# Kernel tuning notes

Hardware: AMD Instinct MI355X
Metric: run time of the kernel (lower is better)

Reference implementation:

```python
import jax, jax.numpy as jnp
import numpy as np
import math

E, NNODE = 32768, 2048          # edges, nodes
NUM_SPECIES, EMB = 100, 32
MUL, HIDDEN, N_RBF, LMAX, ENV_P = 16, 256, 8, 3, 6
SL = {0: slice(0, 1), 1: slice(1, 4), 2: slice(4, 9), 3: slice(9, 16)}  # SH blocks


def _cg(j1, m1, j2, m2, j3, m3):
    """Clebsch-Gordan coefficient (Racah formula), complex SH basis."""
    if m1 + m2 != m3:
        return 0.0
    f = math.factorial
    pre = math.sqrt((2*j3+1) * f(j1+j2-j3) * f(j1-j2+j3) * f(-j1+j2+j3) / f(j1+j2+j3+1))
    pre *= math.sqrt(f(j3+m3)*f(j3-m3)*f(j1-m1)*f(j1+m1)*f(j2-m2)*f(j2+m2))
    s = 0.0
    kmin = max(0, j2 - j3 - m1, j1 - j3 + m2)
    kmax = min(j1 + j2 - j3, j1 - m1, j2 + m2)
    for k in range(kmin, kmax + 1):
        s += (-1)**k / (f(k)*f(j1+j2-j3-k)*f(j1-m1-k)*f(j2+m2-k)*f(j3-j2+m1+k)*f(j3-j1-m2+k))
    return pre * s


def _umat(l):
    """Complex->real spherical-harmonics change of basis."""
    U = np.zeros((2*l+1, 2*l+1), dtype=complex)
    U[l, l] = 1.0
    s2 = 1.0 / math.sqrt(2.0)
    for m in range(1, l + 1):
        U[l+m, l-m] = s2
        U[l+m, l+m] = (-1)**m * s2
        U[l-m, l-m] = 1j * s2
        U[l-m, l+m] = -1j * (-1)**m * s2
    return U


def _real_coupling(l1, l2, l3):
    """Real-basis CG coupling tensor, Frobenius-normalized (w3j analogue)."""
    C = np.zeros((2*l1+1, 2*l2+1, 2*l3+1), dtype=complex)
    for a, m1 in enumerate(range(-l1, l1+1)):
        for b, m2 in enumerate(range(-l2, l2+1)):
            for c, m3 in enumerate(range(-l3, l3+1)):
                C[a, b, c] = _cg(l1, m1, l2, m2, l3, m3)
    T = np.einsum('am,bn,ck,mnk->abc', _umat(l1), _umat(l2), _umat(l3).conj(), C)
    Tr, Ti = np.real(T), np.imag(T)
    T = Tr if np.linalg.norm(Tr) >= np.linalg.norm(Ti) else Ti
    n = np.linalg.norm(T)
    return None if n < 1e-8 else (T / n).astype(np.float32)


PATHS = {l3: [] for l3 in range(LMAX + 1)}
for _l1 in range(LMAX + 1):
    for _l2 in range(LMAX + 1):
        for _l3 in range(abs(_l1 - _l2), min(_l1 + _l2, LMAX) + 1):
            _T = _real_coupling(_l1, _l2, _l3)
            if _T is not None:
                PATHS[_l3].append((_l1, _l2, jnp.asarray(_T)))
NPATH = {l3: len(PATHS[l3]) for l3 in range(LMAX + 1)}


def envelope(d):  # polynomial smoothing envelope, p=6, cutoff=1
    p = ENV_P
    e = 1.0 - 0.5*(p+1)*(p+2)*d**p + p*(p+2)*d**(p+1) - 0.5*p*(p+1)*d**(p+2)
    return jnp.where(d < 1.0, e, 0.0)


def bessel(d):  # radial Bessel basis [E] -> [E, N_RBF]
    n = jnp.arange(1, N_RBF + 1, dtype=d.dtype)
    ds = jnp.where(d == 0.0, 1.0, d)[:, None]
    return (math.sqrt(2.0) * jnp.sin(n * jnp.pi * ds) / ds) * envelope(d)[:, None]


def sph_harm16(u):  # real SH l=0..3, component norm (|Y_l|^2 = 2l+1), [E,16]
    x, y, z = u[:, 0], u[:, 1], u[:, 2]
    x2, y2, z2 = x*x, y*y, z*z
    s3, s15, s5 = math.sqrt(3.0), math.sqrt(15.0), math.sqrt(5.0)
    s358, s105 = math.sqrt(35.0/8.0), math.sqrt(105.0)
    s218, s7 = math.sqrt(21.0/8.0), math.sqrt(7.0)
    return jnp.stack([
        jnp.ones_like(x),
        s3*y, s3*z, s3*x,
        s15*x*y, s15*y*z, 0.5*s5*(3*z2 - 1), s15*x*z, 0.5*s15*(x2 - y2),
        s358*y*(3*x2 - y2), s105*x*y*z, s218*y*(5*z2 - 1), 0.5*s7*(5*z2 - 3)*z,
        s218*x*(5*z2 - 1), 0.5*s105*(x2 - y2)*z, s358*x*(x2 - y2),
    ], axis=1)


def dense(x, W):  # e3nn-style bias-free linear, 1/sqrt(fan_in)
    return (x @ W) / math.sqrt(W.shape[0])


def dense_axis(V, W):  # [E,C,K] x [C,D] -> [E,D,K]
    return jnp.einsum('eck,cd->edk', V, W) / math.sqrt(W.shape[0])


def tensor_product(A, B, lmax_out):
    """CG tensor product [E,MUL,16] x [E,MUL,16] -> {l3: [E,MUL*npath,2l3+1]}."""
    out = {}
    for l3 in range(lmax_out + 1):
        scale = math.sqrt(2*l3 + 1)
        parts = [scale * jnp.einsum('ijk,emi,emj->emk', T, A[:, :, SL[l1]], B[:, :, SL[l2]])
                 for (l1, l2, T) in PATHS[l3]]
        out[l3] = jnp.concatenate(parts, axis=1)
    return out


def allegro_layer(x, V, Y, senders, eps, env, alpha, Ww, Wl, Wv):
    w = dense(x, Ww)                                          # [E,MUL]
    node = jax.ops.segment_sum(w[:, :, None] * Y[:, None, :], senders, num_segments=NNODE)
    wY = node[senders] * eps                                  # scatter_sum + map_back
    lmax_out = LMAX if Wv is not None else 0
    tp = tensor_product(wY, V, lmax_out)
    xc = jnp.concatenate([x, tp[0][:, :, 0]], axis=1)         # fold 0e into scalars
    h = jax.nn.silu(dense(xc, Wl[0]))
    h = jax.nn.silu(dense(h, Wl[1]))
    y = env[:, None] * dense(h, Wl[2])
    a2 = alpha**2
    x = (x + a2 * y) / (1.0 + a2)
    if Wv is None:
        return x, None
    Vn = jnp.concatenate(
        [jnp.zeros((V.shape[0], MUL, 1), x.dtype)] +           # no 0e in output irreps
        [dense_axis(tp[l], Wv[l - 1]) for l in (1, 2, 3)], axis=2)
    return x, Vn


def _forward(vectors, varepsilon, alpha, emb, W_tb1, W_tb2, W_tb3, W_tb4,
             W_w0, W_w1, W_l11, W_l12, W_l13, W_v1, W_v2, W_v3,
             W_w2, W_l21, W_l22, W_l23, W_h, W_out,
             senders, receivers, species):
    d = jnp.linalg.norm(vectors, axis=1)
    u = vectors / jnp.where(d == 0.0, 1.0, d)[:, None]
    env = envelope(d)
    eps = 1.0 / jnp.sqrt(1.0 + varepsilon**2)
    x = jnp.concatenate([bessel(d), emb[species[senders]], emb[species[receivers]]], axis=1)
    x = jnp.where(d[:, None] == 0.0, 0.0, x)
    x = jax.nn.silu(dense(x, W_tb1))
    x = jax.nn.silu(dense(x, W_tb2))
    x = jax.nn.silu(dense(x, W_tb3))
    x = dense(x, W_tb4)
    x = env[:, None] * x                                      # [E,HIDDEN]
    Y = sph_harm16(u)                                         # [E,16]
    V = dense(x, W_w0)[:, :, None] * Y[:, None, :]            # [E,MUL,16]
    x, V = allegro_layer(x, V, Y, senders, eps, env, alpha,
                         W_w1, (W_l11, W_l12, W_l13), (W_v1, W_v2, W_v3))
    x, _ = allegro_layer(x, V, Y, senders, eps, env, alpha,
                         W_w2, (W_l21, W_l22, W_l23), None)
    x = dense(x, W_h)
    return env[:, None] * dense(x, W_out)                     # [E,1]


def setup_inputs():
    key = jax.random.key(0)
    ks = jax.random.split(key, 32)
    dirs = jax.random.normal(ks[0], (E, 3), dtype=jnp.float32)
    dirs = dirs / jnp.linalg.norm(dirs, axis=1, keepdims=True)
    r = jax.random.uniform(ks[1], (E, 1), minval=0.05, maxval=0.95, dtype=jnp.float32)
    w = lambda k, s: jax.random.normal(k, s, dtype=jnp.float32)
    n0 = NPATH[0]
    return {
        "vectors": dirs * r,
        "varepsilon": jnp.asarray(4.0, jnp.float32),   # sqrt(avg_num_neighbors=16)
        "alpha": jnp.asarray(1.0, jnp.float32),
        "emb": w(ks[5], (NUM_SPECIES, EMB)),
        "W_tb1": w(ks[6], (N_RBF + 2*EMB, HIDDEN // 8)),
        "W_tb2": w(ks[7], (HIDDEN // 8, HIDDEN // 4)),
        "W_tb3": w(ks[8], (HIDDEN // 4, HIDDEN // 2)),
        "W_tb4": w(ks[9], (HIDDEN // 2, HIDDEN)),
        "W_w0": w(ks[10], (HIDDEN, MUL)),
        "W_w1": w(ks[11], (HIDDEN, MUL)),
        "W_l11": w(ks[12], (HIDDEN + MUL * n0, HIDDEN)),
        "W_l12": w(ks[13], (HIDDEN, HIDDEN)),
        "W_l13": w(ks[14], (HIDDEN, HIDDEN)),
        "W_v1": w(ks[15], (MUL * NPATH[1], MUL)),
        "W_v2": w(ks[16], (MUL * NPATH[2], MUL)),
        "W_v3": w(ks[17], (MUL * NPATH[3], MUL)),
        "W_w2": w(ks[18], (HIDDEN, MUL)),
        "W_l21": w(ks[19], (HIDDEN + MUL * n0, HIDDEN)),
        "W_l22": w(ks[20], (HIDDEN, HIDDEN)),
        "W_l23": w(ks[21], (HIDDEN, HIDDEN)),
        "W_h": w(ks[22], (HIDDEN, 128)),
        "W_out": w(ks[23], (128, 1)),
        "senders": jax.random.randint(ks[2], (E,), 0, NNODE),
        "receivers": jax.random.randint(ks[3], (E,), 0, NNODE),
        "species": jax.random.randint(ks[4], (NNODE,), 0, NUM_SPECIES),
    }


def reference(vectors, varepsilon, alpha, emb, W_tb1, W_tb2, W_tb3, W_tb4,
              W_w0, W_w1, W_l11, W_l12, W_l13, W_v1, W_v2, W_v3,
              W_w2, W_l21, W_l22, W_l23, W_h, W_out,
              senders, receivers, species):
    return _forward(vectors, varepsilon, alpha, emb, W_tb1, W_tb2, W_tb3, W_tb4,
                    W_w0, W_w1, W_l11, W_l12, W_l13, W_v1, W_v2, W_v3,
                    W_w2, W_l21, W_l22, W_l23, W_h, W_out,
                    senders, receivers, species)
```

## Files before the change

kernel.cpp:

```cpp
#include <hip/hip_runtime.h>
#include <cmath>
#include <complex>
#include <cstdio>
#include <cstring>
#include <algorithm>

#define E_EDGES 32768
#define NNODES  2048
#define VN_E    128

namespace cgt {

static double fct(int n){
  static const double f[13] = {1.,1.,2.,6.,24.,120.,720.,5040.,40320.,362880.,
                               3628800.,39916800.,479001600.};
  return f[n];
}

static double cg(int j1,int m1,int j2,int m2,int j3,int m3){
  if (m1+m2 != m3) return 0.0;
  double pre = std::sqrt((2*j3+1)*fct(j1+j2-j3)*fct(j1-j2+j3)*fct(-j1+j2+j3)/fct(j1+j2+j3+1));
  pre *= std::sqrt(fct(j3+m3)*fct(j3-m3)*fct(j1-m1)*fct(j1+m1)*fct(j2-m2)*fct(j2+m2));
  int kmin = 0;
  if (j2-j3-m1 > kmin) kmin = j2-j3-m1;
// ... 74 lines not shown
};

struct PathTmp {
  int l1,l2,l3, tpoff, kd;
  int ec;
  double T[7][7][7];
};

static void build(Tables& tb){
  static PathTmp paths[40];
  int np = 0, tpoff = 0;
  int l3start[5];
  for (int l3=0;l3<=3;l3++){
    tb.l3base[l3] = tpoff;
    l3start[l3] = np;
    int kd = 2*l3+1;
    for (int l1=0;l1<=3;l1++) for (int l2=0;l2<=3;l2++){
      int lo = (l1>l2)? l1-l2 : l2-l1;
      int hi = std::min(l1+l2,3);
      if (l3 < lo || l3 > hi) continue;
      PathTmp& pt = paths[np];
      if (!realCoupling(l1,l2,l3,pt.T)) continue;
      pt.l1=l1; pt.l2=l2; pt.l3=l3; pt.kd=kd; pt.tpoff=tpoff;
      double scale = std::sqrt((double)kd);
      int cnt = 0;
      for (int a=0;a<2*l1+1;a++)for(int b=0;b<2*l2+1;b++)for(int c=0;c<kd;c++)
        if (std::fabs(pt.T[a][b][c]*scale) > 1e-7) cnt++;
      pt.ec = cnt;
      tpoff += 16*kd;
      np++;
    }
  }
  l3start[4] = np;
  for (int l3=0;l3<=3;l3++) tb.l3np[l3] = l3start[l3+1]-l3start[l3];
  static int order[40];
  for (int i=0;i<np;i++) order[i]=i;
  for (int l3=0;l3<=3;l3++)
    std::sort(order+l3start[l3], order+l3start[l3+1],
              [&](int a,int b){ return paths[a].ec > paths[b].ec; });
  std::memset(tb.TD, 0, sizeof(tb.TD));
  std::memset(tb.pairs, 0, sizeof(tb.pairs));
  static int pmap[16][16];
  for (int i=0;i<16;i++) for (int j=0;j<16;j++) pmap[i][j] = -1;
  int npr = 0;
  int ep = 0;
  for (int slot=0; slot<np; slot++){
    const PathTmp& pt = paths[order[slot]];
    double scale = std::sqrt((double)pt.kd);
    int s1 = pt.l1*pt.l1, s2 = pt.l2*pt.l2;
    tb.pmeta[slot*4+0] = pt.tpoff;
    tb.pmeta[slot*4+1] = ep;
    tb.sl_origc[slot] = ((pt.tpoff - tb.l3base[pt.l3]) / (16*pt.kd)) * 16;
    int tot = 0;
    for (int c=0;c<pt.kd;c++){
      int cnt = 0;
      for (int a=0;a<2*pt.l1+1;a++)for(int b=0;b<2*pt.l2+1;b++){
        double v = pt.T[a][b][c]*scale;
        if (std::fabs(v) > 1e-7){
          tb.val[ep] = (float)v;
          tb.ij[ep]  = (s1+a) | ((s2+b)<<8);
          ep++; cnt++;
          if (pt.l3 >= 1){
            int aa = s1+a, bb = s2+b;
            int pi = pmap[aa][bb];
            if (pi < 0){ pi = npr; pmap[aa][bb] = pi;
                         tb.pairs[npr] = aa | (bb<<8); npr++; }
            tb.TD[(pi*30 + (slot-4))*8 + c] = (float)v;
          }
        }
      }
      tb.ccnt[slot*8+c] = cnt;
      tot += cnt;
    }
    for (int c=pt.kd;c<8;c++) tb.ccnt[slot*8+c]=0;
    tb.pmeta[slot*4+2] = tot;
    tb.pmeta[slot*4+3] = pt.kd;
  }
  if (npr & 1){ tb.pairs[npr] = 0; npr++; }
  tb.npairs = npr;
  tb.npaths = np; tb.nent = ep; tb.tptot = tpoff;
}

}


typedef _Float16 half8 __attribute__((ext_vector_type(8)));
typedef __attribute__((ext_vector_type(4))) float f32x4;

__device__ inline unsigned short f2h(float f){
  union { _Float16 h; unsigned short u; } x;
  x.h = (_Float16)f;
  return x.u;
}
__device__ inline float h2f(unsigned short u){
  union { _Float16 h; unsigned short u; } x; x.u = u;
  return (float)x.h;
}

__device__ inline int swz(int row, int kh){
  int b = row*64 + kh*2;
  return b ^ (((row >> 1) & 3) << 4);
}

__device__ inline float silu(float v){ return v/(1.f+__expf(-v)); }

#define MFMA16 __builtin_amdgcn_mfma_f32_16x16x32_f16

__global__ __launch_bounds__(256) void tb_fused_k(
    const float* __restrict__ X72, const unsigned short* __restrict__ Wt1,
    const unsigned short* __restrict__ Wt2, const unsigned short* __restrict__ Wt3,
    const unsigned short* __restrict__ Wt4, const unsigned short* __restrict__ Wt01,
    const float* __restrict__ Yb, const float* __restrict__ envb,
    unsigned short* __restrict__ Xout, unsigned short* __restrict__ V,
    float* __restrict__ wb)
{
  __shared__ unsigned short AsB[64*32];
  __shared__ unsigned short BsB[256*32];
  __shared__ unsigned short HsA[64*264];
  __shared__ unsigned short HsB[64*264];
  __shared__ float w0s[64*16];
  const int tid  = threadIdx.x;
  const int wave = tid >> 6, lane = tid & 63;
  const int bm = blockIdx.x*64;
  const int mrow = wave*16;
  const int fr = lane & 15, fk = (lane >> 4) * 8;
  const int r4 = (lane >> 4) << 2;
  const int sra = tid >> 2, ska = (tid & 3) * 8;
  const int srb = tid >> 1, skb = (tid & 1) * 16;

  {
    f32x4 acc[2] = {};
    for (int k0 = 0; k0 < 96; k0 += 32) {
      {
        unsigned short u[8];
        int rowg = bm + sra;
#pragma unroll
        for (int q = 0; q < 8; q++) {
          int k = k0 + ska + q;
          u[q] = (k < 72) ? f2h(X72[(size_t)rowg*72 + k]) : (unsigned short)0;
        }
        *(ushort4*)((char*)AsB + swz(sra, ska))     = *(ushort4*)&u[0];
        *(ushort4*)((char*)AsB + swz(sra, ska + 4)) = *(ushort4*)&u[4];
      }
      if (tid < 64) {
        int n = tid >> 1, kb = (tid & 1) * 16;
        unsigned short u[16];
#pragma unroll
        for (int q = 0; q < 16; q++) {
          int k = k0 + kb + q;
          u[q] = (k < 72) ? Wt1[n*72 + k] : (unsigned short)0;
        }
        *(uint4*)((char*)BsB + swz(n, kb))     = *(uint4*)&u[0];
        *(uint4*)((char*)BsB + swz(n, kb + 8)) = *(uint4*)&u[8];
      }
      __syncthreads();
      half8 af = *(half8*)((char*)AsB + swz(mrow + fr, fk));
      half8 b0 = *(half8*)((char*)BsB + swz(fr, fk));
      half8 b1 = *(half8*)((char*)BsB + swz(16 + fr, fk));
      acc[0] = MFMA16(af, b0, acc[0], 0, 0, 0);
      acc[1] = MFMA16(af, b1, acc[1], 0, 0, 0);
      __syncthreads();
    }
    const float rs = 0.11785113019775793f;
#pragma unroll
    for (int j = 0; j < 2; j++)
#pragma unroll
      for (int r = 0; r < 4; r++) {
        int row = mrow + r4 + r;
        HsA[row*264 + j*16 + fr] = f2h(silu(acc[j][r]*rs));
      }
    __syncthreads();
  }

  {
    f32x4 acc[4] = {};
    if (tid < 128) {
      int n = tid >> 1, kb = (tid & 1) * 16;
      const unsigned short* s = Wt2 + n*32 + kb;
      uint4 u0 = *(const uint4*)s;
      uint4 u1 = *(const uint4*)(s + 8);
      *(uint4*)((char*)BsB + swz(n, kb))     = u0;
      *(uint4*)((char*)BsB + swz(n, kb + 8)) = u1;
    }
    __syncthreads();
    half8 af = *(half8*)(HsA + (mrow + fr)*264 + fk);
#pragma unroll
    for (int j = 0; j < 4; j++) {
      half8 bf = *(half8*)((char*)BsB + swz(j*16 + fr, fk));
      acc[j] = MFMA16(af, bf, acc[j], 0, 0, 0);
    }
    __syncthreads();
    const float rs = 0.17677669529663687f;
#pragma unroll
    for (int j = 0; j < 4; j++)
#pragma unroll
      for (int r = 0; r < 4; r++) {
        int row = mrow + r4 + r;
        HsB[row*264 + j*16 + fr] = f2h(silu(acc[j][r]*rs));
      }
    __syncthreads();
  }

  {
    f32x4 acc[8] = {};
    for (int k0 = 0; k0 < 64; k0 += 32) {
      {
        int n = srb, kb = skb;
        const unsigned short* s = Wt3 + n*64 + k0 + kb;
        uint4 u0 = *(const uint4*)s;
        uint4 u1 = *(const uint4*)(s + 8);
        *(uint4*)((char*)BsB + swz(n, kb))     = u0;
        *(uint4*)((char*)BsB + swz(n, kb + 8)) = u1;
      }
      __syncthreads();
      half8 af = *(half8*)(HsB + (mrow + fr)*264 + k0 + fk);
#pragma unroll
      for (int j = 0; j < 8; j++) {
        half8 bf = *(half8*)((char*)BsB + swz(j*16 + fr, fk));
        acc[j] = MFMA16(af, bf, acc[j], 0, 0, 0);
      }
      __syncthreads();
    }
    const float rs = 0.125f;
#pragma unroll
    for (int j = 0; j < 8; j++)
#pragma unroll
      for (int r = 0; r < 4; r++) {
        int row = mrow + r4 + r;
        HsA[row*264 + j*16 + fr] = f2h(silu(acc[j][r]*rs));
      }
    __syncthreads();
  }

  {
    f32x4 acc[16] = {};
    for (int k0 = 0; k0 < 128; k0 += 32) {
#pragma unroll
      for (int h = 0; h < 2; h++) {
        int n = h*128 + srb;
        const unsigned short* s = Wt4 + (size_t)n*128 + k0 + skb;
        uint4 u0 = *(const uint4*)s;
        uint4 u1 = *(const uint4*)(s + 8);
        *(uint4*)((char*)BsB + swz(n, skb))     = u0;
        *(uint4*)((char*)BsB + swz(n, skb + 8)) = u1;
      }
      __syncthreads();
      half8 af = *(half8*)(HsA + (mrow + fr)*264 + k0 + fk);
#pragma unroll
      for (int j = 0; j < 16; j++) {
        half8 bf = *(half8*)((char*)BsB + swz(j*16 + fr, fk));
        acc[j] = MFMA16(af, bf, acc[j], 0, 0, 0);
      }
      __syncthreads();
    }
    const float rs = 0.08838834764831845f;
#pragma unroll
    for (int j = 0; j < 16; j++)
#pragma unroll
      for (int r = 0; r < 4; r++) {
        int row = mrow + r4 + r;
        float v = acc[j][r]*rs*envb[bm + row];
        unsigned short hv = f2h(v);
        HsB[row*264 + j*16 + fr] = hv;
        Xout[((size_t)(bm + row))*256 + j*16 + fr] = hv;
      }
    __syncthreads();
  }

  {
    f32x4 acc[2] = {};
    for (int k0 = 0; k0 < 256; k0 += 32) {
      if (tid < 64) {
        int n = tid >> 1, kb = (tid & 1) * 16;
        const unsigned short* s = Wt01 + (size_t)n*256 + k0 + kb;
        uint4 u0 = *(const uint4*)s;
        uint4 u1 = *(const uint4*)(s + 8);
        *(uint4*)((char*)BsB + swz(n, kb))     = u0;
        *(uint4*)((char*)BsB + swz(n, kb + 8)) = u1;
      }
      __syncthreads();
      half8 af = *(half8*)(HsB + (mrow + fr)*264 + k0 + fk);
      half8 b0 = *(half8*)((char*)BsB + swz(fr, fk));
      half8 b1 = *(half8*)((char*)BsB + swz(16 + fr, fk));
      acc[0] = MFMA16(af, b0, acc[0], 0, 0, 0);
      acc[1] = MFMA16(af, b1, acc[1], 0, 0, 0);
      __syncthreads();
    }
#pragma unroll
    for (int r = 0; r < 4; r++) {
      int row = mrow + r4 + r;
      w0s[row*16 + fr] = acc[0][r]*0.0625f;
      wb[((size_t)(bm + row))*16 + fr] = acc[1][r]*0.0625f;
    }
    __syncthreads();
  }

  for (int i = tid; i < 64*256; i += 256) {
    int e = i >> 8, idx = i & 255;
    V[(((size_t)(bm + e)) << 8) + idx] =
        f2h(w0s[e*16 + (idx & 15)] * Yb[(bm + e)*16 + (idx >> 4)]);
  }
}

__global__ __launch_bounds__(256) void mlp3_k(
    const unsigned short* __restrict__ X, const unsigned short* __restrict__ T0,
    const unsigned short* __restrict__ W1t, const unsigned short* __restrict__ W2t,
    const unsigned short* __restrict__ W3t, unsigned short* __restrict__ Out,
    const float* __restrict__ env, const float* __restrict__ alphap)
{
  __shared__ unsigned short AsB[64*32];
  __shared__ unsigned short BsB[256*32];
  __shared__ unsigned short Hs[64*264];
  const int tid  = threadIdx.x;
  const int wave = tid >> 6, lane = tid & 63;
  const int bm = blockIdx.x*64;
  const int wc = wave*64;
  const int fr = lane & 15, fk = (lane >> 4) * 8;
  const int r4 = (lane >> 4) << 2;
  const int sra = tid >> 2;
  const int ska = (tid & 3) * 8;
  const int srb = tid >> 1;
  const int skb = (tid & 1) * 16;
  f32x4 acc[4][4] = {};

  for (int k0 = 0; k0 < 320; k0 += 32) {
    {
      int kk = k0 + ska;
      const unsigned short* ap = (kk < 256)
        ? X  + (size_t)(bm + sra)*256 + kk
        : T0 + (size_t)(bm + sra)*64  + (kk - 256);
      uint4 u = *(const uint4*)ap;
      *(uint4*)((char*)AsB + swz(sra, ska)) = u;
    }
#pragma unroll
    for (int h = 0; h < 2; h++) {
      int n = h*128 + srb;
      const unsigned short* s = W1t + (size_t)n*320 + k0 + skb;
      uint4 u0 = *(const uint4*)s;
      uint4 u1 = *(const uint4*)(s + 8);
      *(uint4*)((char*)BsB + swz(n, skb))     = u0;
      *(uint4*)((char*)BsB + swz(n, skb + 8)) = u1;
    }
    __syncthreads();
    half8 af[4], bf[4];
#pragma unroll
    for (int i = 0; i < 4; i++)
      af[i] = *(half8*)((char*)AsB + swz(i*16 + fr, fk));
#pragma unroll
    for (int j = 0; j < 4; j++)
      bf[j] = *(half8*)((char*)BsB + swz(wc + j*16 + fr, fk));
#pragma unroll
    for (int i = 0; i < 4; i++)
#pragma unroll
      for (int j = 0; j < 4; j++)
        acc[i][j] = MFMA16(af[i], bf[j], acc[i][j], 0, 0, 0);
    __syncthreads();
  }
  const float rs320 = 0.055901699437494740f;
#pragma unroll
  for (int i = 0; i < 4; i++)
#pragma unroll
    for (int r = 0; r < 4; r++) {
      int row = i*16 + r4 + r;
#pragma unroll
      for (int j = 0; j < 4; j++) {
        int col = wc + j*16 + fr;
        Hs[row*264 + col] = f2h(silu(acc[i][j][r]*rs320));
        acc[i][j][r] = 0.f;
      }
    }
  __syncthreads();

  for (int k0 = 0; k0 < 256; k0 += 32) {
#pragma unroll
    for (int h = 0; h < 2; h++) {
      int n = h*128 + srb;
      const unsigned short* s = W2t + (size_t)n*256 + k0 + skb;
      uint4 u0 = *(const uint4*)s;
      uint4 u1 = *(const uint4*)(s + 8);
      *(uint4*)((char*)BsB + swz(n, skb))     = u0;
      *(uint4*)((char*)BsB + swz(n, skb + 8)) = u1;
    }
    __syncthreads();
    half8 af[4], bf[4];
#pragma unroll
    for (int i = 0; i < 4; i++)
      af[i] = *(half8*)(Hs + (i*16 + fr)*264 + k0 + fk);
#pragma unroll
    for (int j = 0; j < 4; j++)
      bf[j] = *(half8*)((char*)BsB + swz(wc + j*16 + fr, fk));
#pragma unroll
    for (int i = 0; i < 4; i++)
#pragma unroll
      for (int j = 0; j < 4; j++)
        acc[i][j] = MFMA16(af[i], bf[j], acc[i][j], 0, 0, 0);
    __syncthreads();
  }
#pragma unroll
  for (int i = 0; i < 4; i++)
#pragma unroll
    for (int r = 0; r < 4; r++) {
      int row = i*16 + r4 + r;
#pragma unroll
      for (int j = 0; j < 4; j++) {
        int col = wc + j*16 + fr;
        Hs[row*264 + col] = f2h(silu(acc[i][j][r]*0.0625f));
        acc[i][j][r] = 0.f;
      }
    }
  __syncthreads();

  for (int k0 = 0; k0 < 256; k0 += 32) {
#pragma unroll
    for (int h = 0; h < 2; h++) {
      int n = h*128 + srb;
      const unsigned short* s = W3t + (size_t)n*256 + k0 + skb;
      uint4 u0 = *(const uint4*)s;
      uint4 u1 = *(const uint4*)(s + 8);
      *(uint4*)((char*)BsB + swz(n, skb))     = u0;
      *(uint4*)((char*)BsB + swz(n, skb + 8)) = u1;
    }
    __syncthreads();
    half8 af[4], bf[4];
#pragma unroll
    for (int i = 0; i < 4; i++)
      af[i] = *(half8*)(Hs + (i*16 + fr)*264 + k0 + fk);
#pragma unroll
    for (int j = 0; j < 4; j++)
      bf[j] = *(half8*)((char*)BsB + swz(wc + j*16 + fr, fk));
#pragma unroll
    for (int i = 0; i < 4; i++)
#pragma unroll
      for (int j = 0; j < 4; j++)
        acc[i][j] = MFMA16(af[i], bf[j], acc[i][j], 0, 0, 0);
    __syncthreads();
  }
  float al = alphap[0];
  float a2 = al*al, inv1a2 = 1.f/(1.f+a2);
#pragma unroll
  for (int i = 0; i < 4; i++)
#pragma unroll
    for (int r = 0; r < 4; r++) {
      int row = bm + i*16 + r4 + r;
      float ev = env[row];
#pragma unroll
      for (int j = 0; j < 4; j++) {
        int col = wc + j*16 + fr;
        float v = acc[i][j][r]*0.0625f*ev;
        v = (h2f(X[(size_t)row*256+col]) + a2*v)*inv1a2;
        Out[(size_t)row*256+col] = f2h(v);
      }
    }
}

__global__ __launch_bounds__(512) void vn_k(
    const float* __restrict__ node, const unsigned short* __restrict__ V,
    const int* __restrict__ senders, const float* __restrict__ varepsp,
    const int* __restrict__ pairsG, const unsigned short* __restrict__ Gtt,
    unsigned short* __restrict__ Vn, int Kdim,
    const int* __restrict__ pmeta, const int* __restrict__ entIJ,
    const float* __restrict__ entVal, unsigned short* __restrict__ tp0)
{
  __shared__ unsigned short Ab[VN_E*264];
  __shared__ unsigned short Bb[VN_E*264];
  __shared__ int Ps[256];
  const int tid = threadIdx.x;
  const int e0 = blockIdx.x * VN_E;
  const int wave = tid >> 6, lane = tid & 63;
  float ve = varepsp[0];
  float eps = rsqrtf(1.f + ve*ve);
  if (tid < 256) Ps[tid] = pairsG[tid];
#pragma unroll
  for (int rr = 0; rr < 16; rr++) {
    int row = wave*16 + rr;
    int s = senders[e0 + row];
    float4 fa = *(const float4*)(node + ((size_t)s << 8) + 4*lane);
    uint2 ub = *(const uint2*)(V + (((size_t)(e0 + row)) << 8) + 4*lane);
    unsigned short* ad = Ab + row*264 + 4*lane;
    unsigned short* bd = Bb + row*264 + 4*lane;
    uint2 ua;
    ua.x = (unsigned)f2h(fa.x*eps) | ((unsigned)f2h(fa.y*eps) << 16);
    ua.y = (unsigned)f2h(fa.z*eps) | ((unsigned)f2h(fa.w*eps) << 16);
    *(uint2*)ad = ua;
    *(uint2*)bd = ub;
  }
  __syncthreads();
  for (int o = tid; o < VN_E*64; o += 512) {
    int e = o >> 6, c = o & 63;
    int p = c >> 4, m = c & 15;
    const unsigned short* Ae = Ab + e*264;
    const unsigned short* Be = Bb + e*264;
    int es = pmeta[p*4+1], ec = pmeta[p*4+2];
    float acc = 0.f;
    for (int t = 0; t < ec; t++) {
      int ij = entIJ[es+t];
      acc += entVal[es+t] * h2f(Ae[((ij&255)<<4)+m]) * h2f(Be[(((ij>>8)&255)<<4)+m]);
    }
    tp0[((size_t)(e0+e)<<6) + pmeta[p*4+0] + m] = f2h(acc);
  }
  const int rowb = (wave & 1) * 64;
  const int wc   = (wave >> 1) * 64;
  const int fr = lane & 15, fk = (lane >> 4) * 8;
  const int pairSel = fk >> 4;
  const int moff = fk & 15;
  const int nslab = Kdim >> 5;
  f32x4 acc[4][4] = {};

  const unsigned short* Ar0 = Ab + (rowb + fr)*264;
  const unsigned short* Br0 = Bb + (rowb + fr)*264;
  const unsigned short* Ar1 = Ab + (rowb + 16 + fr)*264;
  const unsigned short* Br1 = Bb + (rowb + 16 + fr)*264;
  const unsigned short* Ar2 = Ab + (rowb + 32 + fr)*264;
  const unsigned short* Br2 = Bb + (rowb + 32 + fr)*264;
  const unsigned short* Ar3 = Ab + (rowb + 48 + fr)*264;
  const unsigned short* Br3 = Bb + (rowb + 48 + fr)*264;

  const unsigned short* gp = Gtt + ((size_t)(wc + fr)) * 32 + fk;
  half8 b0 = *(const half8*)(gp);
  half8 b1 = *(const half8*)(gp + 512);
  half8 b2 = *(const half8*)(gp + 1024);
  half8 b3 = *(const half8*)(gp + 1536);
  half8 c0 = b0, c1 = b1, c2 = b2, c3 = b3;
  if (nslab > 1) {
    const unsigned short* g1 = gp + 8192;
    c0 = *(const half8*)(g1);
    c1 = *(const half8*)(g1 + 512);
    c2 = *(const half8*)(g1 + 1024);
    c3 = *(const half8*)(g1 + 1536);
  }
  int p0 = Ps[pairSel];
  int aoff = ((p0 & 255) << 4) + moff;
  int boff = (((p0 >> 8) & 255) << 4) + moff;
  half8 rA0 = *(const half8*)(Ar0 + aoff);
  half8 rB0 = *(const half8*)(Br0 + boff);
  half8 rA1 = *(const half8*)(Ar1 + aoff);
  half8 rB1 = *(const half8*)(Br1 + boff);
  half8 rA2 = *(const half8*)(Ar2 + aoff);
  half8 rB2 = *(const half8*)(Br2 + boff);
  half8 rA3 = *(const half8*)(Ar3 + aoff);
  half8 rB3 = *(const half8*)(Br3 + boff);

  for (int sl = 0; sl < nslab; sl++) {
    half8 a0 = rA0 * rB0;
    half8 a1 = rA1 * rB1;
    half8 a2 = rA2 * rB2;
    half8 a3 = rA3 * rB3;
    if (sl + 1 < nslab) {
      int pn = Ps[2*(sl + 1) + pairSel];
      int aoffn = ((pn & 255) << 4) + moff;
      int boffn = (((pn >> 8) & 255) << 4) + moff;
      rA0 = *(const half8*)(Ar0 + aoffn);
      rB0 = *(const half8*)(Br0 + boffn);
      rA1 = *(const half8*)(Ar1 + aoffn);
      rB1 = *(const half8*)(Br1 + boffn);
      rA2 = *(const half8*)(Ar2 + aoffn);
      rB2 = *(const half8*)(Br2 + boffn);
      rA3 = *(const half8*)(Ar3 + aoffn);
      rB3 = *(const half8*)(Br3 + boffn);
    }
    half8 d0, d1, d2, d3;
    if (sl + 2 < nslab) {
      const unsigned short* gn = gp + (size_t)(sl + 2) * 8192;
      d0 = *(const half8*)(gn);
      d1 = *(const half8*)(gn + 512);
      d2 = *(const half8*)(gn + 1024);
      d3 = *(const half8*)(gn + 1536);
    } else { d0 = c0; d1 = c1; d2 = c2; d3 = c3; }
    acc[0][0] = MFMA16(a0, b0, acc[0][0], 0, 0, 0);
    acc[1][0] = MFMA16(a1, b0, acc[1][0], 0, 0, 0);
    acc[2][0] = MFMA16(a2, b0, acc[2][0], 0, 0, 0);
    acc[3][0] = MFMA16(a3, b0, acc[3][0], 0, 0, 0);
    acc[0][1] = MFMA16(a0, b1, acc[0][1], 0, 0, 0);
    acc[1][1] = MFMA16(a1, b1, acc[1][1], 0, 0, 0);
    acc[2][1] = MFMA16(a2, b1, acc[2][1], 0, 0, 0);
    acc[3][1] = MFMA16(a3, b1, acc[3][1], 0, 0, 0);
    acc[0][2] = MFMA16(a0, b2, acc[0][2], 0, 0, 0);
    acc[1][2] = MFMA16(a1, b2, acc[1][2], 0, 0, 0);
    acc[2][2] = MFMA16(a2, b2, acc[2][2], 0, 0, 0);
    acc[3][2] = MFMA16(a3, b2, acc[3][2], 0, 0, 0);
    acc[0][3] = MFMA16(a0, b3, acc[0][3], 0, 0, 0);
    acc[1][3] = MFMA16(a1, b3, acc[1][3], 0, 0, 0);
    acc[2][3] = MFMA16(a2, b3, acc[2][3], 0, 0, 0);
    acc[3][3] = MFMA16(a3, b3, acc[3][3], 0, 0, 0);
    b0 = c0; b1 = c1; b2 = c2; b3 = c3;
    c0 = d0; c1 = d1; c2 = d2; c3 = d3;
  }
  const int r4 = (lane >> 4) << 2;
#pragma unroll
  for (int rg = 0; rg < 4; rg++) {
#pragma unroll
    for (int j = 0; j < 4; j++) {
#pragma unroll
      for (int r = 0; r < 4; r++) {
        int row = e0 + rowb + rg*16 + r4 + r;
        int col = wc + j*16 + fr;
        Vn[(size_t)row*256 + col] = f2h(acc[rg][j][r]);
      }
    }
  }
}

__global__ void gbuild_k(const float* __restrict__ TD,
    const float* __restrict__ Wv1, const float* __restrict__ Wv2,
    const float* __restrict__ Wv3, const int* __restrict__ sl_origc,
    unsigned short* __restrict__ Gt, int Kdim, int npairs,
    int s1b, int s1e, int s2e, int s3e)
{
  int k = blockIdx.x*256 + threadIdx.x;
  if (k >= Kdim) return;
  int col = blockIdx.y;
  int pair = k >> 4, m = k & 15;
  int d = col & 15, kabs = col >> 4;
  float acc = 0.f;
  if (kabs > 0 && pair < npairs) {
    const float* Wv; int ss, se, kloc;
    if (kabs < 4)      { Wv = Wv1; ss = s1b; se = s1e; kloc = kabs - 1; }
    else if (kabs < 9) { Wv = Wv2; ss = s1e; se = s2e; kloc = kabs - 4; }
    else               { Wv = Wv3; ss = s2e; se = s3e; kloc = kabs - 9; }
    for (int slot = ss; slot < se; slot++)
      acc += TD[((pair*30) + (slot - 4))*8 + kloc] * Wv[(sl_origc[slot] + m)*16 + d];
    acc *= rsqrtf((float)(16*(se - ss)));
  }
  Gt[((size_t)((k >> 5)*256 + col))*32 + (k & 31)] = f2h(acc);
}

struct WDesc { const float* src; unsigned short* dst; int K; int lgN; };
struct WPack { WDesc d[10]; };
__global__ void wcvt_k(WPack p){
  WDesc d = p.d[blockIdx.y];
  int total = d.K << d.lgN;
  int gid = blockIdx.x*256 + threadIdx.x;
  if (gid >= total) return;
  int k = gid >> d.lgN, n = gid & ((1 << d.lgN) - 1);
  d.dst[(size_t)n*d.K + k] = f2h(d.src[gid]);
}

__global__ void wcvt01_k(const float* __restrict__ W0, const float* __restrict__ W1,
                         unsigned short* __restrict__ dst){
  int gid = blockIdx.x*256 + threadIdx.x;
  int k = gid >> 5, n = gid & 31;
  float v = (n < 16) ? W0[k*16 + n] : W1[k*16 + (n - 16)];
  dst[(size_t)n*256 + k] = f2h(v);
}

__global__ void whc_k(const float* __restrict__ Wh, const float* __restrict__ Wout,
                      float* __restrict__ hc)
{
  int k = threadIdx.x;
  float s = 0.f;
#pragma unroll 16
  for (int j = 0; j < 128; j++) s += Wh[k*128 + j] * Wout[j];
  hc[k] = s;
}

__global__ void final256_k(const unsigned short* __restrict__ X,
    const float* __restrict__ hc, const float* __restrict__ env,
    float* __restrict__ out)
{
  const int e = blockIdx.x*256 + threadIdx.x;
  float acc = 0.f;
#pragma unroll 16
  for (int k = 0; k < 256; k++) acc += h2f(X[((size_t)e<<8)+k])*hc[k];
  out[e] = env[e]*acc*0.0055242717280199023f;
}

__global__ __launch_bounds__(256) void dense16_k(const unsigned short* __restrict__ A,
    const float* __restrict__ W, float* __restrict__ C)
{
  __shared__ float As[16*256];
  const int r0 = blockIdx.x << 4;
  const int tid = threadIdx.x;
  for (int i = tid; i < 16*256; i += 256)
    As[i] = h2f(A[((size_t)r0<<8) + i]);
  __syncthreads();
  const int r = tid >> 4, n = tid & 15;
  float acc = 0.f;
#pragma unroll 8
  for (int k = 0; k < 256; k++)
    acc += As[(r<<8)+k] * W[(k<<4)+n];
  C[((size_t)(r0+r)<<4)+n] = acc * 0.0625f;
}

__global__ void edge_init_k(const float* __restrict__ vectors, const int* __restrict__ senders,
    const int* __restrict__ receivers, const int* __restrict__ species,
    const float* __restrict__ emb, float* __restrict__ envb, float* __restrict__ Yb,
    float* __restrict__ x72)
{
  const int e = blockIdx.x*256 + threadIdx.x;
  float vx = vectors[e*3+0], vy = vectors[e*3+1], vz = vectors[e*3+2];
  float d = sqrtf(vx*vx+vy*vy+vz*vz);
  float dd = (d==0.f) ? 1.f : d;
  float invd = 1.f/dd;
  float x = vx*invd, y = vy*invd, z = vz*invd;
  float d2=d*d, d3=d2*d, d6=d3*d3, d7=d6*d, d8=d7*d;
  float envv = (d<1.f) ? (1.f - 28.f*d6 + 48.f*d7 - 21.f*d8) : 0.f;
  envb[e] = envv;
  float mask = (d==0.f)?0.f:1.f;
  const float SQ2 = 1.41421356237309515f;
  const float PIf = 3.14159265358979323846f;
  float* xr = x72 + (size_t)e*72;
#pragma unroll
  for (int n=1;n<=8;n++)
    xr[n-1] = SQ2 * sinf((float)n*PIf*dd)*invd*envv*mask;
  int sp_s = species[senders[e]], sp_r = species[receivers[e]];
  const float* es_ = emb + (size_t)sp_s*32;
  const float* er_ = emb + (size_t)sp_r*32;
#pragma unroll 8
  for (int k=0;k<32;k++){ xr[8+k] = es_[k]*mask; xr[40+k] = er_[k]*mask; }
  float x2=x*x, y2=y*y, z2=z*z;
  const float s3=1.7320508075688772f, s15=3.872983346207417f, s5=2.23606797749979f;
  const float s358=2.0916500663351889f, s105=10.246950765959598f;
  const float s218=1.6201851746019651f, s7=2.6457513110645907f;
  float* Yr = Yb + ((size_t)e<<4);
  Yr[0]=1.f;           Yr[1]=s3*y;          Yr[2]=s3*z;           Yr[3]=s3*x;
  Yr[4]=s15*x*y;       Yr[5]=s15*y*z;       Yr[6]=0.5f*s5*(3.f*z2-1.f);
  Yr[7]=s15*x*z;       Yr[8]=0.5f*s15*(x2-y2);
  Yr[9]=s358*y*(3.f*x2-y2);  Yr[10]=s105*x*y*z;  Yr[11]=s218*y*(5.f*z2-1.f);
  Yr[12]=0.5f*s7*(5.f*z2-3.f)*z;  Yr[13]=s218*x*(5.f*z2-1.f);
  Yr[14]=0.5f*s105*(x2-y2)*z;     Yr[15]=s358*x*(x2-y2);
}

__global__ void hist_k(const int* __restrict__ senders, int* cnt){
  int e = blockIdx.x*256 + threadIdx.x;
  atomicAdd(&cnt[senders[e]], 1);
}

__global__ void scan_k(const int* __restrict__ cnt, int* __restrict__ starts,
                       int* __restrict__ cursor){
  __shared__ int s[NNODES];
  const int tid = threadIdx.x;
  for (int i = tid; i < NNODES; i += 256) s[i] = cnt[i];
  __syncthreads();
  if (tid == 0) {
    int run = 0;
    for (int i = 0; i < NNODES; i++) { int c = s[i]; s[i] = run; run += c; }
  }
  __syncthreads();
  for (int i = tid; i < NNODES; i += 256) { starts[i] = s[i]; cursor[i] = s[i]; }
  if (tid == 0) starts[NNODES] = E_EDGES;
}

__global__ void perm_k(const int* __restrict__ senders, int* cursor,
                       int* __restrict__ perm){
  int e = blockIdx.x*256 + threadIdx.x;
  int pos = atomicAdd(&cursor[senders[e]], 1);
  perm[pos] = e;
}

__global__ __launch_bounds__(256) void nodesum_k(const float* __restrict__ w,
    const float* __restrict__ Y, const int* __restrict__ perm,
    const int* __restrict__ starts, float* __restrict__ node)
{
  __shared__ float buf[8*32];
  const int n = blockIdx.x;
  const int tid = threadIdx.x;
  const int s0 = starts[n], s1 = starts[n+1];
  const int a = tid >> 4, m = tid & 15;
  float acc = 0.f;
  for (int i = s0; i < s1; i += 8) {
    int nb = s1 - i; if (nb > 8) nb = 8;
    int slot = tid >> 5, comp = tid & 31;
    if (slot < nb) {
      int e = perm[i + slot];
      buf[slot*32 + comp] = (comp < 16) ? w[(e<<4)+comp] : Y[(e<<4)+comp-16];
    }
    __syncthreads();
    for (int q = 0; q < nb; q++)
      acc += buf[q*32 + m] * buf[q*32 + 16 + a];
    __syncthreads();
  }
  node[((size_t)n<<8) + tid] = acc;
}

__global__ void tp2_k(const float* __restrict__ node, const unsigned short* __restrict__ Vn,
    const int* __restrict__ senders, const float* __restrict__ varepsp,
    const int* __restrict__ pmeta, const int* __restrict__ entIJ,
    const float* __restrict__ entVal, unsigned short* __restrict__ tp0)
{
  const int gid = blockIdx.x*256 + threadIdx.x;
  const int e = gid >> 6, c = gid & 63;
  const int p = c >> 4, m = c & 15;
  float ve = varepsp[0];
  float eps = rsqrtf(1.f + ve*ve);
  int s = senders[e];
  const float* Am = &node[((size_t)s<<8)];
  const unsigned short* Bm = &Vn[((size_t)e<<8)];
  int es = pmeta[p*4+1], ec = pmeta[p*4+2];
  float acc = 0.f;
  for (int t=0;t<ec;t++){
    int ij = entIJ[es+t];
    acc += entVal[es+t] * Am[((ij&255)<<4) + m] * h2f(Bm[(((ij>>8)&255)<<4) + m]);
  }
  tp0[((size_t)e<<6) + pmeta[p*4+0] + m] = f2h(acc * eps);
}


extern "C" void kernel_launch(void* const* d_in, const int* in_sizes, int n_in,
                              void* d_out, int out_size, void* d_ws, size_t ws_size,
                              hipStream_t stream)
{
  const float* vectors = (const float*)d_in[0];
  const float* vareps  = (const float*)d_in[1];
  const float* alpha   = (const float*)d_in[2];
  const float* emb     = (const float*)d_in[3];
  const float* W_tb1   = (const float*)d_in[4];
  const float* W_tb2   = (const float*)d_in[5];
  const float* W_tb3   = (const float*)d_in[6];
  const float* W_tb4   = (const float*)d_in[7];
  const float* W_w0    = (const float*)d_in[8];
  const float* W_w1    = (const float*)d_in[9];
  const float* W_l11   = (const float*)d_in[10];
  const float* W_l12   = (const float*)d_in[11];
  const float* W_l13   = (const float*)d_in[12];
  const float* W_v1    = (const float*)d_in[13];
  const float* W_v2    = (const float*)d_in[14];
  const float* W_v3    = (const float*)d_in[15];
  const float* W_w2    = (const float*)d_in[16];
  const float* W_l21   = (const float*)d_in[17];
  const float* W_l22   = (const float*)d_in[18];
  const float* W_l23   = (const float*)d_in[19];
  const float* W_h     = (const float*)d_in[20];
  const float* W_out   = (const float*)d_in[21];
  const int* senders   = (const int*)d_in[22];
  const int* receivers = (const int*)d_in[23];
  const int* species   = (const int*)d_in[24];

  static cgt::Tables tb;
  cgt::build(tb);
  const int Kdim = tb.npairs * 16;

  char* ws = (char*)d_ws;
  size_t off = 0;
  auto alloc = [&](size_t bytes)->void*{
    void* p = ws + off; off += (bytes + 255) & ~(size_t)255; return p;
  };
  float* t_val = (float*)alloc(sizeof(tb.val));
  int*   t_ij  = (int*)  alloc(sizeof(tb.ij));
  int*   t_pm  = (int*)  alloc(sizeof(tb.pmeta));
  float* t_td  = (float*)alloc(sizeof(tb.TD));
  int*   t_pr  = (int*)  alloc(sizeof(tb.pairs));
  int*   t_oc  = (int*)  alloc(sizeof(tb.sl_origc));
  float* envb  = (float*)alloc((size_t)E_EDGES*4);
  float* Yb    = (float*)alloc((size_t)E_EDGES*16*4);
  float* xb    = (float*)alloc((size_t)E_EDGES*256*4);
  float* Vb    = (float*)alloc((size_t)E_EDGES*256*4);
  float* bufA  = (float*)alloc((size_t)E_EDGES*72*4);
  float* wb    = (float*)alloc((size_t)E_EDGES*16*4);
  float* tp0b  = (float*)alloc((size_t)E_EDGES*64*4);
  float* nodeb = (float*)alloc((size_t)NNODES*256*4);
  float* hcb   = (float*)alloc(256*4);
  int* cntb    = (int*)alloc(NNODES*4);
  int* startsb = (int*)alloc((NNODES+1)*4);
  int* cursorb = (int*)alloc(NNODES*4);
  int* permb   = (int*)alloc(E_EDGES*4);
  unsigned short* Gt = (unsigned short*)alloc((size_t)256*Kdim*2);
  unsigned short* Wt_tb1 = (unsigned short*)alloc(32*72*2);
  unsigned short* Wt_tb2 = (unsigned short*)alloc(64*32*2);
  unsigned short* Wt_tb3 = (unsigned short*)alloc(128*64*2);
  unsigned short* Wt_tb4 = (unsigned short*)alloc(256*128*2);
  unsigned short* Wt_w01 = (unsigned short*)alloc(32*256*2);
  unsigned short* Wt_l11 = (unsigned short*)alloc(320*256*2);
  unsigned short* Wt_l12 = (unsigned short*)alloc(256*256*2);
  unsigned short* Wt_l13 = (unsigned short*)alloc(256*256*2);
  unsigned short* Wt_l21 = (unsigned short*)alloc(320*256*2);
  unsigned short* Wt_l22 = (unsigned short*)alloc(256*256*2);
  unsigned short* Wt_l23 = (unsigned short*)alloc(256*256*2);
  if (off > ws_size) {
    fprintf(stderr, "[allegro] workspace too small: need %zu, have %zu\n", off, ws_size);
    return;
  }
  unsigned short* xb16 = (unsigned short*)xb;
  unsigned short* tp016 = (unsigned short*)tp0b;
  unsigned short* V16 = (unsigned short*)Vb;

  hipMemcpyAsync(t_val, tb.val,     sizeof(tb.val),     hipMemcpyHostToDevice, stream);
  hipMemcpyAsync(t_ij,  tb.ij,      sizeof(tb.ij),      hipMemcpyHostToDevice, stream);
  hipMemcpyAsync(t_pm,  tb.pmeta,   sizeof(tb.pmeta),   hipMemcpyHostToDevice, stream);
  hipMemcpyAsync(t_td,  tb.TD,      sizeof(tb.TD),      hipMemcpyHostToDevice, stream);
  hipMemcpyAsync(t_pr,  tb.pairs,   sizeof(tb.pairs),   hipMemcpyHostToDevice, stream);
  hipMemcpyAsync(t_oc,  tb.sl_origc,sizeof(tb.sl_origc),hipMemcpyHostToDevice, stream);

  const int s1b = tb.l3np[0];
  const int s1e = s1b + tb.l3np[1];
  const int s2e = s1e + tb.l3np[2];
  const int s3e = s2e + tb.l3np[3];

  {
    dim3 g((Kdim + 255)/256, 256);
    gbuild_k<<<g, 256, 0, stream>>>(t_td, W_v1, W_v2, W_v3, t_oc, Gt, Kdim,
                                    tb.npairs, s1b, s1e, s2e, s3e);
  }
  {
    WPack p;
    p.d[0] = { W_tb1, Wt_tb1,  72, 5 };
    p.d[1] = { W_tb2, Wt_tb2,  32, 6 };
    p.d[2] = { W_tb3, Wt_tb3,  64, 7 };
    p.d[3] = { W_tb4, Wt_tb4, 128, 8 };
    p.d[4] = { W_l11, Wt_l11, 320, 8 };
    p.d[5] = { W_l12, Wt_l12, 256, 8 };
    p.d[6] = { W_l13, Wt_l13, 256, 8 };
    p.d[7] = { W_l21, Wt_l21, 320, 8 };
    p.d[8] = { W_l22, Wt_l22, 256, 8 };
    p.d[9] = { W_l23, Wt_l23, 256, 8 };
    dim3 g(320, 10);
    wcvt_k<<<g, 256, 0, stream>>>(p);
  }
  wcvt01_k<<<32, 256, 0, stream>>>(W_w0, W_w1, Wt_w01);
  whc_k<<<1, 256, 0, stream>>>(W_h, W_out, hcb);

  hipMemsetAsync(cntb, 0, NNODES*4, stream);
  hist_k<<<E_EDGES/256, 256, 0, stream>>>(senders, cntb);
  scan_k<<<1, 256, 0, stream>>>(cntb, startsb, cursorb);
  perm_k<<<E_EDGES/256, 256, 0, stream>>>(senders, cursorb, permb);

  edge_init_k<<<E_EDGES/256, 256, 0, stream>>>(vectors, senders, receivers, species,
                                               emb, envb, Yb, bufA);
  tb_fused_k<<<E_EDGES/64, 256, 0, stream>>>(bufA, Wt_tb1, Wt_tb2, Wt_tb3, Wt_tb4,
                                             Wt_w01, Yb, envb, xb16, V16, wb);

  nodesum_k<<<NNODES, 256, 0, stream>>>(wb, Yb, permb, startsb, nodeb);
  vn_k<<<E_EDGES/VN_E, 512, 0, stream>>>(nodeb, V16, senders, vareps, t_pr, Gt,
                                         V16, Kdim, t_pm, t_ij, t_val, tp016);
  mlp3_k<<<E_EDGES/64, 256, 0, stream>>>(xb16, tp016, Wt_l11, Wt_l12, Wt_l13,
                                         xb16, envb, alpha);

  dense16_k<<<E_EDGES/16, 256, 0, stream>>>(xb16, W_w2, wb);
  nodesum_k<<<NNODES, 256, 0, stream>>>(wb, Yb, permb, startsb, nodeb);
  tp2_k<<<E_EDGES*64/256, 256, 0, stream>>>(nodeb, V16, senders, vareps, t_pm, t_ij,
                                            t_val, tp016);
  mlp3_k<<<E_EDGES/64, 256, 0, stream>>>(xb16, tp016, Wt_l21, Wt_l22, Wt_l23,
                                         xb16, envb, alpha);

  final256_k<<<E_EDGES/256, 256, 0, stream>>>(xb16, hcb, envb, (float*)d_out);
}
```

Baseline: 405.0 us.

## Fuse W_w2 projection and final readout into 128-row, 512-thread mlp3 kernels

The edge MLP kernel now handles 128 rows per block with 8 waves, so each weight tile staged in shared memory serves twice as many rows. A template mode fuses the following step into its epilogue: mode 0 runs the W_w2 projection with MFMA on the result held in shared memory, and mode 1 computes the final per-edge energy dot product and skips writing the second layer's output. This removes the separate dense16 and final256 kernels and one full read of the edge feature matrix, and mode 1 also drops one full write. The cost is more shared memory per block, which may lower occupancy, and an epilogue where only some waves do the small W_w2 GEMM.

```diff
diff --git a/kernel.cpp b/kernel.cpp
--- a/kernel.cpp
+++ b/kernel.cpp
@@ -400,25 +400,30 @@
   }
 }
 
-__global__ __launch_bounds__(256) void mlp3_k(
+template<int MODE>
+__global__ __launch_bounds__(512) void mlp3_k(
     const unsigned short* __restrict__ X, const unsigned short* __restrict__ T0,
     const unsigned short* __restrict__ W1t, const unsigned short* __restrict__ W2t,
     const unsigned short* __restrict__ W3t, unsigned short* __restrict__ Out,
-    const float* __restrict__ env, const float* __restrict__ alphap)
+    const float* __restrict__ env, const float* __restrict__ alphap,
+    const unsigned short* __restrict__ Wtw2, float* __restrict__ wb,
+    const float* __restrict__ hc, float* __restrict__ outE)
 {
-  __shared__ unsigned short AsB[64*32];
+  __shared__ unsigned short AsB[128*32];
   __shared__ unsigned short BsB[256*32];
-  __shared__ unsigned short Hs[64*264];
+  __shared__ unsigned short Hs[128*264];
+  __shared__ float hcs[256];
+  __shared__ float red[512];
   const int tid  = threadIdx.x;
   const int wave = tid >> 6, lane = tid & 63;
-  const int bm = blockIdx.x*64;
-  const int wc = wave*64;
+  const int bm = blockIdx.x*128;
+  const int rowh = (wave >> 2)*64;
+  const int wc = (wave & 3)*64;
   const int fr = lane & 15, fk = (lane >> 4) * 8;
   const int r4 = (lane >> 4) << 2;
-  const int sra = tid >> 2;
-  const int ska = (tid & 3) * 8;
-  const int srb = tid >> 1;
-  const int skb = (tid & 1) * 16;
+  const int sra = tid >> 2, ska = (tid & 3) * 8;
+  const int srb = tid >> 1, skb = (tid & 1) * 16;
+  if (MODE == 1 && tid < 256) hcs[tid] = hc[tid];
   f32x4 acc[4][4] = {};
 
   for (int k0 = 0; k0 < 320; k0 += 32) {
@@ -427,23 +432,18 @@
       const unsigned short* ap = (kk < 256)
         ? X  + (size_t)(bm + sra)*256 + kk
         : T0 + (size_t)(bm + sra)*64  + (kk - 256);
-      uint4 u = *(const uint4*)ap;
-      *(uint4*)((char*)AsB + swz(sra, ska)) = u;
-    }
-#pragma unroll
-    for (int h = 0; h < 2; h++) {
-      int n = h*128 + srb;
-      const unsigned short* s = W1t + (size_t)n*320 + k0 + skb;
-      uint4 u0 = *(const uint4*)s;
-      uint4 u1 = *(const uint4*)(s + 8);
-      *(uint4*)((char*)BsB + swz(n, skb))     = u0;
-      *(uint4*)((char*)BsB + swz(n, skb + 8)) = u1;
+      *(uint4*)((char*)AsB + swz(sra, ska)) = *(const uint4*)ap;
+    }
+    {
+      const unsigned short* s = W1t + (size_t)srb*320 + k0 + skb;
+      *(uint4*)((char*)BsB + swz(srb, skb))     = *(const uint4*)s;
+      *(uint4*)((char*)BsB + swz(srb, skb + 8)) = *(const uint4*)(s + 8);
     }
     __syncthreads();
     half8 af[4], bf[4];
 #pragma unroll
     for (int i = 0; i < 4; i++)
-      af[i] = *(half8*)((char*)AsB + swz(i*16 + fr, fk));
+      af[i] = *(half8*)((char*)AsB + swz(rowh + i*16 + fr, fk));
 #pragma unroll
     for (int j = 0; j < 4; j++)
       bf[j] = *(half8*)((char*)BsB + swz(wc + j*16 + fr, fk));
@@ -459,31 +459,26 @@
   for (int i = 0; i < 4; i++)
 #pragma unroll
     for (int r = 0; r < 4; r++) {
-      int row = i*16 + r4 + r;
+      int row = rowh + i*16 + r4 + r;
 #pragma unroll
       for (int j = 0; j < 4; j++) {
-        int col = wc + j*16 + fr;
-        Hs[row*264 + col] = f2h(silu(acc[i][j][r]*rs320));
+        Hs[row*264 + wc + j*16 + fr] = f2h(silu(acc[i][j][r]*rs320));
         acc[i][j][r] = 0.f;
       }
     }
   __syncthreads();
 
   for (int k0 = 0; k0 < 256; k0 += 32) {
-#pragma unroll
-    for (int h = 0; h < 2; h++) {
-      int n = h*128 + srb;
-      const unsigned short* s = W2t + (size_t)n*256 + k0 + skb;
-      uint4 u0 = *(const uint4*)s;
-      uint4 u1 = *(const uint4*)(s + 8);
-      *(uint4*)((char*)BsB + swz(n, skb))     = u0;
-      *(uint4*)((char*)BsB + swz(n, skb + 8)) = u1;
+    {
+      const unsigned short* s = W2t + (size_t)srb*256 + k0 + skb;
+      *(uint4*)((char*)BsB + swz(srb, skb))     = *(const uint4*)s;
+      *(uint4*)((char*)BsB + swz(srb, skb + 8)) = *(const uint4*)(s + 8);
     }
     __syncthreads();
     half8 af[4], bf[4];
 #pragma unroll
     for (int i = 0; i < 4; i++)
-      af[i] = *(half8*)(Hs + (i*16 + fr)*264 + k0 + fk);
+      af[i] = *(half8*)(Hs + (rowh + i*16 + fr)*264 + k0 + fk);
 #pragma unroll
     for (int j = 0; j < 4; j++)
       bf[j] = *(half8*)((char*)BsB + swz(wc + j*16 + fr, fk));
@@ -498,31 +493,26 @@
   for (int i = 0; i < 4; i++)
 #pragma unroll
     for (int r = 0; r < 4; r++) {
-      int row = i*16 + r4 + r;
+      int row = rowh + i*16 + r4 + r;
 #pragma unroll
       for (int j = 0; j < 4; j++) {
-        int col = wc + j*16 + fr;
-        Hs[row*264 + col] = f2h(silu(acc[i][j][r]*0.0625f));
+        Hs[row*264 + wc + j*16 + fr] = f2h(silu(acc[i][j][r]*0.0625f));
         acc[i][j][r] = 0.f;
       }
     }
   __syncthreads();
 
   for (int k0 = 0; k0 < 256; k0 += 32) {
-#pragma unroll
-    for (int h = 0; h < 2; h++) {
-      int n = h*128 + srb;
-      const unsigned short* s = W3t + (size_t)n*256 + k0 + skb;
-      uint4 u0 = *(const uint4*)s;
-      uint4 u1 = *(const uint4*)(s + 8);
-      *(uint4*)((char*)BsB + swz(n, skb))     = u0;
-      *(uint4*)((char*)BsB + swz(n, skb + 8)) = u1;
+    {
+      const unsigned short* s = W3t + (size_t)srb*256 + k0 + skb;
+      *(uint4*)((char*)BsB + swz(srb, skb))     = *(const uint4*)s;
+      *(uint4*)((char*)BsB + swz(srb, skb + 8)) = *(const uint4*)(s + 8);
     }
     __syncthreads();
     half8 af[4], bf[4];
 #pragma unroll
     for (int i = 0; i < 4; i++)
-      af[i] = *(half8*)(Hs + (i*16 + fr)*264 + k0 + fk);
+      af[i] = *(half8*)(Hs + (rowh + i*16 + fr)*264 + k0 + fk);
 #pragma unroll
     for (int j = 0; j < 4; j++)
       bf[j] = *(half8*)((char*)BsB + swz(wc + j*16 + fr, fk));
@@ -533,22 +523,69 @@
         acc[i][j] = MFMA16(af[i], bf[j], acc[i][j], 0, 0, 0);
     __syncthreads();
   }
-  float al = alphap[0];
-  float a2 = al*al, inv1a2 = 1.f/(1.f+a2);
-#pragma unroll
-  for (int i = 0; i < 4; i++)
-#pragma unroll
-    for (int r = 0; r < 4; r++) {
-      int row = bm + i*16 + r4 + r;
-      float ev = env[row];
-#pragma unroll
-      for (int j = 0; j < 4; j++) {
-        int col = wc + j*16 + fr;
-        float v = acc[i][j][r]*0.0625f*ev;
-        v = (h2f(X[(size_t)row*256+col]) + a2*v)*inv1a2;
-        Out[(size_t)row*256+col] = f2h(v);
-      }
-    }
+  {
+    float al = alphap[0];
+    float a2 = al*al, inv1a2 = 1.f/(1.f+a2);
+#pragma unroll
+    for (int i = 0; i < 4; i++)
+#pragma unroll
+      for (int r = 0; r < 4; r++) {
+        int row = rowh + i*16 + r4 + r;
+        int grow = bm + row;
+        float ev = env[grow];
+#pragma unroll
+        for (int j = 0; j < 4; j++) {
+          int col = wc + j*16 + fr;
+          float v = acc[i][j][r]*0.0625f*ev;
+          v = (h2f(X[(size_t)grow*256 + col]) + a2*v)*inv1a2;
+          unsigned short hv = f2h(v);
+          Hs[row*264 + col] = hv;
+          if (MODE == 0) Out[(size_t)grow*256 + col] = hv;
+        }
+      }
+  }
+  __syncthreads();
+
+  if (MODE == 0) {
+    f32x4 acc2[4] = {};
+    for (int k0 = 0; k0 < 256; k0 += 32) {
+      if (tid < 32) {
+        int n = tid >> 1, kb = (tid & 1) * 16;
+        const unsigned short* s = Wtw2 + (size_t)n*256 + k0 + kb;
+        *(uint4*)((char*)BsB + swz(n, kb))     = *(const uint4*)s;
+        *(uint4*)((char*)BsB + swz(n, kb + 8)) = *(const uint4*)(s + 8);
+      }
+      __syncthreads();
+      if ((wave & 3) == 0) {
+        half8 bf = *(half8*)((char*)BsB + swz(fr, fk));
+#pragma unroll
+        for (int i = 0; i < 4; i++) {
+          half8 af = *(half8*)(Hs + (rowh + i*16 + fr)*264 + k0 + fk);
+          acc2[i] = MFMA16(af, bf, acc2[i], 0, 0, 0);
+        }
+      }
+      __syncthreads();
+    }
+    if ((wave & 3) == 0) {
+#pragma unroll
+      for (int i = 0; i < 4; i++)
+#pragma unroll
+        for (int r = 0; r < 4; r++)
+          wb[((size_t)(bm + rowh + i*16 + r4 + r))*16 + fr] = acc2[i][r]*0.0625f;
+    }
+  } else {
+    int row = tid >> 2, q = tid & 3;
+    float p = 0.f;
+#pragma unroll 16
+    for (int c = q*64; c < q*64 + 64; c++)
+      p += h2f(Hs[row*264 + c]) * hcs[c];
+    red[tid] = p;
+    __syncthreads();
+    if (q == 0) {
+      float t = red[tid] + red[tid+1] + red[tid+2] + red[tid+3];
+      outE[bm + row] = env[bm + row]*t*0.0055242717280199023f;
+    }
+  }
 }
 
 __global__ __launch_bounds__(512) void vn_k(
@@ -723,7 +760,7 @@
 }
 
 struct WDesc { const float* src; unsigned short* dst; int K; int lgN; };
-struct WPack { WDesc d[10]; };
+struct WPack { WDesc d[11]; };
 __global__ void wcvt_k(WPack p){
   WDesc d = p.d[blockIdx.y];
   int total = d.K << d.lgN;
@@ -749,34 +786,6 @@
 #pragma unroll 16
   for (int j = 0; j < 128; j++) s += Wh[k*128 + j] * Wout[j];
   hc[k] = s;
-}
-
-__global__ void final256_k(const unsigned short* __restrict__ X,
-    const float* __restrict__ hc, const float* __restrict__ env,
-    float* __restrict__ out)
-{
-  const int e = blockIdx.x*256 + threadIdx.x;
-  float acc = 0.f;
-#pragma unroll 16
-  for (int k = 0; k < 256; k++) acc += h2f(X[((size_t)e<<8)+k])*hc[k];
-  out[e] = env[e]*acc*0.0055242717280199023f;
-}
-
-__global__ __launch_bounds__(256) void dense16_k(const unsigned short* __restrict__ A,
-    const float* __restrict__ W, float* __restrict__ C)
-{
-  __shared__ float As[16*256];
-  const int r0 = blockIdx.x << 4;
-  const int tid = threadIdx.x;
-  for (int i = tid; i < 16*256; i += 256)
-    As[i] = h2f(A[((size_t)r0<<8) + i]);
-  __syncthreads();
-  const int r = tid >> 4, n = tid & 15;
-  float acc = 0.f;
-#pragma unroll 8
-  for (int k = 0; k < 256; k++)
-    acc += As[(r<<8)+k] * W[(k<<4)+n];
-  C[((size_t)(r0+r)<<4)+n] = acc * 0.0625f;
 }
 
 __global__ void edge_init_k(const float* __restrict__ vectors, const int* __restrict__ senders,
@@ -957,6 +966,7 @@
   unsigned short* Wt_tb3 = (unsigned short*)alloc(128*64*2);
   unsigned short* Wt_tb4 = (unsigned short*)alloc(256*128*2);
   unsigned short* Wt_w01 = (unsigned short*)alloc(32*256*2);
+  unsigned short* Wt_w2  = (unsigned short*)alloc(16*256*2);
   unsigned short* Wt_l11 = (unsigned short*)alloc(320*256*2);
   unsigned short* Wt_l12 = (unsigned short*)alloc(256*256*2);
   unsigned short* Wt_l13 = (unsigned short*)alloc(256*256*2);
@@ -990,17 +1000,18 @@
   }
   {
     WPack p;
-    p.d[0] = { W_tb1, Wt_tb1,  72, 5 };
-    p.d[1] = { W_tb2, Wt_tb2,  32, 6 };
-    p.d[2] = { W_tb3, Wt_tb3,  64, 7 };
-    p.d[3] = { W_tb4, Wt_tb4, 128, 8 };
-    p.d[4] = { W_l11, Wt_l11, 320, 8 };
-    p.d[5] = { W_l12, Wt_l12, 256, 8 };
-    p.d[6] = { W_l13, Wt_l13, 256, 8 };
-    p.d[7] = { W_l21, Wt_l21, 320, 8 };
-    p.d[8] = { W_l22, Wt_l22, 256, 8 };
-    p.d[9] = { W_l23, Wt_l23, 256, 8 };
-    dim3 g(320, 10);
+    p.d[0]  = { W_tb1, Wt_tb1,  72, 5 };
+    p.d[1]  = { W_tb2, Wt_tb2,  32, 6 };
+    p.d[2]  = { W_tb3, Wt_tb3,  64, 7 };
+    p.d[3]  = { W_tb4, Wt_tb4, 128, 8 };
+    p.d[4]  = { W_l11, Wt_l11, 320, 8 };
+    p.d[5]  = { W_l12, Wt_l12, 256, 8 };
+    p.d[6]  = { W_l13, Wt_l13, 256, 8 };
+    p.d[7]  = { W_l21, Wt_l21, 320, 8 };
+    p.d[8]  = { W_l22, Wt_l22, 256, 8 };
+    p.d[9]  = { W_l23, Wt_l23, 256, 8 };
+    p.d[10] = { W_w2,  Wt_w2,  256, 4 };
+    dim3 g(320, 11);
     wcvt_k<<<g, 256, 0, stream>>>(p);
   }
   wcvt01_k<<<32, 256, 0, stream>>>(W_w0, W_w1, Wt_w01);
@@ -1019,15 +1030,14 @@
   nodesum_k<<<NNODES, 256, 0, stream>>>(wb, Yb, permb, startsb, nodeb);
   vn_k<<<E_EDGES/VN_E, 512, 0, stream>>>(nodeb, V16, senders, vareps, t_pr, Gt,
                                          V16, Kdim, t_pm, t_ij, t_val, tp016);
-  mlp3_k<<<E_EDGES/64, 256, 0, stream>>>(xb16, tp016, Wt_l11, Wt_l12, Wt_l13,
-                                         xb16, envb, alpha);
-
-  dense16_k<<<E_EDGES/16, 256, 0, stream>>>(xb16, W_w2, wb);
+  mlp3_k<0><<<E_EDGES/128, 512, 0, stream>>>(xb16, tp016, Wt_l11, Wt_l12, Wt_l13,
+                                             xb16, envb, alpha, Wt_w2, wb,
+                                             nullptr, nullptr);
+
   nodesum_k<<<NNODES, 256, 0, stream>>>(wb, Yb, permb, startsb, nodeb);
   tp2_k<<<E_EDGES*64/256, 256, 0, stream>>>(nodeb, V16, senders, vareps, t_pm, t_ij,
                                             t_val, tp016);
-  mlp3_k<<<E_EDGES/64, 256, 0, stream>>>(xb16, tp016, Wt_l21, Wt_l22, Wt_l23,
-                                         xb16, envb, alpha);
-
-  final256_k<<<E_EDGES/256, 256, 0, stream>>>(xb16, hcb, envb, (float*)d_out);
-}
+  mlp3_k<1><<<E_EDGES/128, 512, 0, stream>>>(xb16, tp016, Wt_l21, Wt_l22, Wt_l23,
+                                             nullptr, envb, alpha, nullptr, nullptr,
+                                             hcb, (float*)d_out);
+}
```

New measurement: 388.0 us. 4.2% less time.
